# Kernel optimization log

Measured on AMD Instinct MI355X. Metric: run time of the kernel, lower is better.

## Reference

```python
import jax, jax.numpy as jnp
import numpy as np

N = 100000      # nodes
E = 1600000     # edges
D_IN, D_H, D_OUT = 256, 64, 47


def setup_inputs() -> dict:
    key = jax.random.key(0)
    k0, k1, k2, k3 = jax.random.split(key, 4)
    x = jax.random.normal(k0, (N, D_IN), dtype=jnp.float32)
    edge_index = jax.random.randint(k1, (2, E), 0, N, dtype=jnp.int64)
    W1 = jax.random.normal(k2, (D_IN, D_H), dtype=jnp.float32) / np.sqrt(D_IN)
    b1 = jnp.zeros((D_H,), dtype=jnp.float32)
    W2 = jax.random.normal(k3, (D_H, D_OUT), dtype=jnp.float32) / np.sqrt(D_H)
    b2 = jnp.zeros((D_OUT,), dtype=jnp.float32)
    return {"x": x, "edge_index": edge_index, "W1": W1, "b1": b1, "W2": W2, "b2": b2}


def _gcn_conv(x, W, b, src, dst, norm):
    # PyG GCNConv: h = x @ W, then scatter_add(norm * h[src] -> dst), + bias
    h = x @ W                                     # [N, out]
    msg = norm[:, None] * h[src]                  # [E+N, out] gather
    out = jax.ops.segment_sum(msg, dst, num_segments=N)  # scatter-add
    return out + b


def reference(x, edge_index, W1, b1, W2, b2):
    # add self-loops with weight 1 (PyG default, edge_weight=None -> ones)
    loop = jnp.arange(N, dtype=edge_index.dtype)
    src = jnp.concatenate([edge_index[0], loop])
    dst = jnp.concatenate([edge_index[1], loop])
    w = jnp.ones((E + N,), dtype=x.dtype)
    # symmetric normalization: deg^-1/2[src] * w * deg^-1/2[dst]
    deg = jax.ops.segment_sum(w, dst, num_segments=N)
    dinv = jnp.where(deg > 0, jax.lax.rsqrt(deg), 0.0)
    norm = dinv[src] * w * dinv[dst]              # [E+N]

    h = _gcn_conv(x, W1, b1, src, dst, norm)
    h = jax.nn.relu(h)
    # F.dropout(training=self.training): eval mode -> identity
    xo = _gcn_conv(h, W2, b2, src, dst, norm)     # [N, D_OUT]
    logits = jax.nn.softmax(xo, axis=1)           # nn.Softmax() -> dim=1 for 2D
    preds = jnp.argmax(logits, axis=1)
    return (logits, preds, xo)
```

## Files before the change

kernel.cpp:

```cpp
#include <hip/hip_runtime.h>
#include <math.h>

#define NN 100000
#define NE 1600000
#define DI 256
#define DH 64
#define DO 47
#define DH3 48
#define NB ((NN + 255) / 256)
#define RSZ8 ((NN + 7) / 8)
#define EPB 2048
#define CPB ((NE + EPB - 1) / EPB)

typedef float f8 __attribute__((ext_vector_type(8)));

__global__ __launch_bounds__(256) void k_degree(const int* __restrict__ dst,
                                                int* __restrict__ deg) {
    int r = blockIdx.x & 7;
    int chunk = blockIdx.x >> 3;
    int lo = r * RSZ8, hi = min(lo + RSZ8, NN);
    int base = chunk * EPB + threadIdx.x;
    #pragma unroll
    for (int i = 0; i < EPB / 256; ++i) {
        int e = base + i * 256;
        if (e < NE) {
            int d = dst[e];
            if (d >= lo && d < hi) atomicAdd(&deg[d], 1);
        }
    }
}

__global__ __launch_bounds__(256) void k_part(const int* __restrict__ deg,
                                              int* __restrict__ part) {
    int i = blockIdx.x * 256 + threadIdx.x;
    int v = (i < NN) ? deg[i] : 0;
    for (int off = 32; off; off >>= 1) v += __shfl_xor(v, off);
    __shared__ int s[4];
    if ((threadIdx.x & 63) == 0) s[threadIdx.x >> 6] = v;
    __syncthreads();
    if (threadIdx.x == 0) part[blockIdx.x] = s[0] + s[1] + s[2] + s[3];
}

__global__ __launch_bounds__(512) void k_scanpart(int* __restrict__ part) {
    int t = threadIdx.x, lane = t & 63, wv = t >> 6;
    int v0 = (t < NB) ? part[t] : 0;
    int v = v0;
    for (int off = 1; off < 64; off <<= 1) {
        int u = __shfl_up(v, off);
        if (lane >= off) v += u;
    }
    __shared__ int ws[8];
    if (lane == 63) ws[wv] = v;
    __syncthreads();
    if (t == 0) {
        int run = 0;
        for (int w = 0; w < 8; ++w) { int tmp = ws[w]; ws[w] = run; run += tmp; }
    }
    __syncthreads();
    v += ws[wv];
    if (t < NB) part[t] = v - v0;
}

__global__ __launch_bounds__(256) void k_scan3(const int* __restrict__ deg,
                                               const int* __restrict__ part,
                                               int* __restrict__ rowptr,
                                               int* __restrict__ cursor,
                                               float* __restrict__ dinv) {
    int i = blockIdx.x * 256 + threadIdx.x;
    int lane = threadIdx.x & 63, wv = threadIdx.x >> 6;
    int v0 = (i < NN) ? deg[i] : 0;
    int v = v0;
    for (int off = 1; off < 64; off <<= 1) {
        int u = __shfl_up(v, off);
        if (lane >= off) v += u;
    }
    __shared__ int ws[4], wo[4];
    if (lane == 63) ws[wv] = v;
    __syncthreads();
    if (threadIdx.x == 0) {
        int run = 0;
        for (int w = 0; w < 4; ++w) { int tmp = ws[w]; wo[w] = run; run += tmp; }
    }
    __syncthreads();
    int excl = part[blockIdx.x] + wo[wv] + v - v0;
    if (i < NN) {
        rowptr[i] = excl;
        cursor[i] = excl;
        dinv[i] = rsqrtf((float)(v0 + 1));
    }
}

__global__ __launch_bounds__(256) void k_fillr(const int* __restrict__ src,
                                               const int* __restrict__ dst,
                                               int* __restrict__ cursor,
                                               int* __restrict__ csr_src) {
    int r = blockIdx.x & 7;
    int chunk = blockIdx.x >> 3;
    int lo = r * RSZ8, hi = min(lo + RSZ8, NN);
    int base = chunk * EPB + threadIdx.x;
    #pragma unroll
    for (int i = 0; i < EPB / 256; ++i) {
        int e = base + i * 256;
        if (e < NE) {
            int d = dst[e];
            if (d >= lo && d < hi) {
                int p = atomicAdd(&cursor[d], 1);
                csr_src[p] = src[e];
            }
        }
    }
}

__global__ __launch_bounds__(512) void k_gemm1(const float* __restrict__ x,
                                               const float* __restrict__ W1,
                                               const float* __restrict__ dinv,
                                               float* __restrict__ h1s) {
    __shared__ float xs[2][64 * 33];
    const int t = threadIdx.x;
    const int lane = t & 63;
    const int wvu = __builtin_amdgcn_readfirstlane(t >> 6);
    const int r0 = blockIdx.x * 64;
    const int sr = t >> 3;
    const int sk = (t & 7) * 4;
    const long xrow = (long)min(r0 + sr, NN - 1) * DI;
    const int row = r0 + lane;

    float acc[8] = {0.f, 0.f, 0.f, 0.f, 0.f, 0.f, 0.f, 0.f};

    {
        float4 v = *(const float4*)(x + xrow + sk);
        float* p = &xs[0][sr * 33 + sk];
        p[0] = v.x; p[1] = v.y; p[2] = v.z; p[3] = v.w;
    }
    __syncthreads();
    for (int c = 0; c < 8; ++c) {
        const int buf = c & 1;
        if (c + 1 < 8) {
            float4 v = *(const float4*)(x + xrow + (c + 1) * 32 + sk);
            float* p = &xs[buf ^ 1][sr * 33 + sk];
            p[0] = v.x; p[1] = v.y; p[2] = v.z; p[3] = v.w;
        }
        const f8* wp = (const f8*)(W1) + (size_t)(c * 32) * (DH / 8) + wvu;
        #pragma unroll
        for (int k = 0; k < 32; ++k) {
            float xv = xs[buf][lane * 33 + k];
            f8 w8 = wp[(size_t)k * (DH / 8)];
            #pragma unroll
            for (int j = 0; j < 8; ++j) acc[j] += w8[j] * xv;
        }
        __syncthreads();
    }
    if (row < NN) {
        float di = dinv[row];
        float4 o0 = {di * acc[0], di * acc[1], di * acc[2], di * acc[3]};
        float4 o1 = {di * acc[4], di * acc[5], di * acc[6], di * acc[7]};
        float4* hp = (float4*)(h1s + (long)row * DH + wvu * 8);
        hp[0] = o0;
        hp[1] = o1;
    }
}

__global__ __launch_bounds__(256) void k_agg1(const int* __restrict__ rowptr,
                                              const int* __restrict__ deg,
                                              const int* __restrict__ csr_src,
                                              const float* __restrict__ dinv,
                                              const float* __restrict__ h1s,
                                              const float* __restrict__ b1,
                                              const float* __restrict__ W2,
                                              float* __restrict__ h3s) {
    __shared__ float w2[DH * DO];
    __shared__ float sh[8][DH];
    for (int i = threadIdx.x; i < DH * DO; i += 256) w2[i] = W2[i];
    __syncthreads();
    const int wv = threadIdx.x >> 6, lane = threadIdx.x & 63;
    const int rA = blockIdx.x * 8 + wv * 2;
    const int rB = rA + 1;
    const int begA = rowptr[rA], cntA = deg[rA];
    const int begB = rowptr[rB], cntB = deg[rB];
    float accA = 0.f, accB = 0.f;
    const int tmax = max(cntA, cntB);
    #pragma unroll 2
    for (int j = 0; j < tmax; j += 4) {
        #pragma unroll
        for (int k = 0; k < 4; ++k) {
            int sa = csr_src[min(begA + j + k, NE - 1)];
            int sb = csr_src[min(begB + j + k, NE - 1)];
            float va = h1s[(size_t)sa * DH + lane];
            float vb = h1s[(size_t)sb * DH + lane];
            accA += (j + k < cntA) ? va : 0.f;
            accB += (j + k < cntB) ? vb : 0.f;
        }
    }
    const float diA = dinv[rA], diB = dinv[rB];
    float vA = diA * (accA + h1s[(size_t)rA * DH + lane]) + b1[lane];
    float vB = diB * (accB + h1s[(size_t)rB * DH + lane]) + b1[lane];
    sh[wv * 2 + 0][lane] = fmaxf(vA, 0.f);
    sh[wv * 2 + 1][lane] = fmaxf(vB, 0.f);
    __syncthreads();
    if (lane < DO) {
        float oA = 0.f, oB = 0.f;
        #pragma unroll 8
        for (int k = 0; k < DH; ++k) {
            float w = w2[k * DO + lane];
            oA += sh[wv * 2 + 0][k] * w;
            oB += sh[wv * 2 + 1][k] * w;
        }
        h3s[(size_t)rA * DH3 + lane] = diA * oA;
        h3s[(size_t)rB * DH3 + lane] = diB * oB;
    }
}

__global__ __launch_bounds__(256) void k_agg2(const int* __restrict__ rowptr,
                                              const int* __restrict__ deg,
                                              const int* __restrict__ csr_src,
                                              const float* __restrict__ dinv,
                                              const float* __restrict__ h3s,
                                              const float* __restrict__ b2,
                                              float* __restrict__ logits,
                                              float* __restrict__ preds,
                                              float* __restrict__ xo) {
    const int wv = threadIdx.x >> 6, lane = threadIdx.x & 63;
    const int rA = blockIdx.x * 8 + wv * 2;
    const int rB = rA + 1;
    const int begA = rowptr[rA], cntA = deg[rA];
    const int begB = rowptr[rB], cntB = deg[rB];
    const bool act = lane < DO;
    const int lx = act ? lane : 0;
    float accA = 0.f, accB = 0.f;
    const int tmax = max(cntA, cntB);
    #pragma unroll 2
    for (int j = 0; j < tmax; j += 4) {
        #pragma unroll
        for (int k = 0; k < 4; ++k) {
            int sa = csr_src[min(begA + j + k, NE - 1)];
            int sb = csr_src[min(begB + j + k, NE - 1)];
            float va = h3s[(size_t)sa * DH3 + lx];
            float vb = h3s[(size_t)sb * DH3 + lx];
            accA += (j + k < cntA) ? va : 0.f;
            accB += (j + k < cntB) ? vb : 0.f;
        }
    }
    const float diA = dinv[rA], diB = dinv[rB];
    float valA = -INFINITY, valB = -INFINITY;
    if (act) {
        valA = diA * (accA + h3s[(size_t)rA * DH3 + lane]) + b2[lane];
        valB = diB * (accB + h3s[(size_t)rB * DH3 + lane]) + b2[lane];
        xo[(size_t)rA * DO + lane] = valA;
        xo[(size_t)rB * DO + lane] = valB;
    }
    float mA = valA, mB = valB;
    for (int off = 32; off; off >>= 1) {
        mA = fmaxf(mA, __shfl_xor(mA, off));
        mB = fmaxf(mB, __shfl_xor(mB, off));
    }
    int idxA = (act && valA == mA) ? lane : (1 << 30);
    int idxB = (act && valB == mB) ? lane : (1 << 30);
    for (int off = 32; off; off >>= 1) {
        idxA = min(idxA, __shfl_xor(idxA, off));
        idxB = min(idxB, __shfl_xor(idxB, off));
    }
    float evA = act ? expf(valA - mA) : 0.f;
    float evB = act ? expf(valB - mB) : 0.f;
    float sA = evA, sB = evB;
    for (int off = 32; off; off >>= 1) {
        sA += __shfl_xor(sA, off);
        sB += __shfl_xor(sB, off);
    }
    if (act) {
        logits[(size_t)rA * DO + lane] = evA / sA;
        logits[(size_t)rB * DO + lane] = evB / sB;
    }
    if (lane == 0) {
        preds[rA] = (float)idxA;
        preds[rB] = (float)idxB;
    }
}

extern "C" void kernel_launch(void* const* d_in, const int* in_sizes, int n_in,
                              void* d_out, int out_size, void* d_ws, size_t ws_size,
                              hipStream_t stream) {
    const float* x  = (const float*)d_in[0];
    const int*   ei = (const int*)d_in[1];
    const float* W1 = (const float*)d_in[2];
    const float* b1 = (const float*)d_in[3];
    const float* W2 = (const float*)d_in[4];
    const float* b2 = (const float*)d_in[5];
    const int* src = ei;
    const int* dst = ei + NE;

    float* out    = (float*)d_out;
    float* logits = out;
    float* preds  = out + (size_t)NN * DO;
    float* xo     = preds + NN;

    char* wsb = (char*)d_ws;
    int*   deg     = (int*)wsb;                         wsb += (size_t)NN * 4;
    float* dinv    = (float*)wsb;                       wsb += (size_t)NN * 4;
    int*   rowptr  = (int*)wsb;                         wsb += (size_t)NN * 4;
    int*   cursor  = (int*)wsb;                         wsb += (size_t)NN * 4;
    int*   part    = (int*)wsb;                         wsb += (size_t)512 * 4;
    int*   csr_src = (int*)wsb;                         wsb += (size_t)NE * 4;
    float* h1s     = (float*)wsb;                       wsb += (size_t)NN * DH * 4;
    float* h3s     = (float*)wsb;                       wsb += (size_t)NN * DH3 * 4;

    hipMemsetAsync(deg, 0, NN * sizeof(int), stream);

    k_degree<<<8 * CPB, 256, 0, stream>>>(dst, deg);
    k_part<<<NB, 256, 0, stream>>>(deg, part);
    k_scanpart<<<1, 512, 0, stream>>>(part);
    k_scan3<<<NB, 256, 0, stream>>>(deg, part, rowptr, cursor, dinv);
    k_fillr<<<8 * CPB, 256, 0, stream>>>(src, dst, cursor, csr_src);
    k_gemm1<<<(NN + 63) / 64, 512, 0, stream>>>(x, W1, dinv, h1s);
    k_agg1<<<NN / 8, 256, 0, stream>>>(rowptr, deg, csr_src, dinv, h1s, b1, W2, h3s);
    k_agg2<<<NN / 8, 256, 0, stream>>>(rowptr, deg, csr_src, dinv, h3s, b2, logits, preds, xo);
}
```

Measured before the change: 347.0 us.

## Stage W1 tiles in LDS and process four rows per wave in aggregations

The GEMM kernel now double-buffers 32x64 tiles of W1 in shared memory alongside the x tiles, replacing per-wave global vector loads of the weights. The two aggregation kernels now handle four destination rows per wave instead of two, which puts more independent gathers in flight and amortizes the per-block W2 staging over more rows. The costs are extra LDS use, higher register pressure and more load imbalance between rows of different degree within a wave.

```diff
diff --git a/kernel.cpp b/kernel.cpp
--- a/kernel.cpp
+++ b/kernel.cpp
@@ -116,12 +116,15 @@
                                                const float* __restrict__ dinv,
                                                float* __restrict__ h1s) {
     __shared__ float xs[2][64 * 33];
+    __shared__ float wl[2][32 * 64];
     const int t = threadIdx.x;
     const int lane = t & 63;
     const int wvu = __builtin_amdgcn_readfirstlane(t >> 6);
     const int r0 = blockIdx.x * 64;
     const int sr = t >> 3;
     const int sk = (t & 7) * 4;
+    const int wk = t >> 4;
+    const int wc = (t & 15) * 4;
     const long xrow = (long)min(r0 + sr, NN - 1) * DI;
     const int row = r0 + lane;
 
@@ -131,6 +134,9 @@
         float4 v = *(const float4*)(x + xrow + sk);
         float* p = &xs[0][sr * 33 + sk];
         p[0] = v.x; p[1] = v.y; p[2] = v.z; p[3] = v.w;
+        float4 w = *(const float4*)(W1 + (size_t)wk * DH + wc);
+        float* q = &wl[0][wk * 64 + wc];
+        q[0] = w.x; q[1] = w.y; q[2] = w.z; q[3] = w.w;
     }
     __syncthreads();
     for (int c = 0; c < 8; ++c) {
@@ -139,12 +145,14 @@
             float4 v = *(const float4*)(x + xrow + (c + 1) * 32 + sk);
             float* p = &xs[buf ^ 1][sr * 33 + sk];
             p[0] = v.x; p[1] = v.y; p[2] = v.z; p[3] = v.w;
-        }
-        const f8* wp = (const f8*)(W1) + (size_t)(c * 32) * (DH / 8) + wvu;
+            float4 w = *(const float4*)(W1 + (size_t)((c + 1) * 32 + wk) * DH + wc);
+            float* q = &wl[buf ^ 1][wk * 64 + wc];
+            q[0] = w.x; q[1] = w.y; q[2] = w.z; q[3] = w.w;
+        }
         #pragma unroll
         for (int k = 0; k < 32; ++k) {
             float xv = xs[buf][lane * 33 + k];
-            f8 w8 = wp[(size_t)k * (DH / 8)];
+            f8 w8 = *(const f8*)&wl[buf][k * 64 + wvu * 8];
             #pragma unroll
             for (int j = 0; j < 8; ++j) acc[j] += w8[j] * xv;
         }
@@ -169,44 +177,49 @@
                                               const float* __restrict__ W2,
                                               float* __restrict__ h3s) {
     __shared__ float w2[DH * DO];
-    __shared__ float sh[8][DH];
+    __shared__ float sh[16][DH];
     for (int i = threadIdx.x; i < DH * DO; i += 256) w2[i] = W2[i];
     __syncthreads();
     const int wv = threadIdx.x >> 6, lane = threadIdx.x & 63;
-    const int rA = blockIdx.x * 8 + wv * 2;
-    const int rB = rA + 1;
-    const int begA = rowptr[rA], cntA = deg[rA];
-    const int begB = rowptr[rB], cntB = deg[rB];
-    float accA = 0.f, accB = 0.f;
-    const int tmax = max(cntA, cntB);
-    #pragma unroll 2
+    const int rbase = blockIdx.x * 16 + wv * 4;
+    int beg[4], cnt[4];
+    float acc[4] = {0.f, 0.f, 0.f, 0.f};
+    #pragma unroll
+    for (int r = 0; r < 4; ++r) {
+        beg[r] = rowptr[rbase + r];
+        cnt[r] = deg[rbase + r];
+    }
+    const int tmax = max(max(cnt[0], cnt[1]), max(cnt[2], cnt[3]));
     for (int j = 0; j < tmax; j += 4) {
         #pragma unroll
         for (int k = 0; k < 4; ++k) {
-            int sa = csr_src[min(begA + j + k, NE - 1)];
-            int sb = csr_src[min(begB + j + k, NE - 1)];
-            float va = h1s[(size_t)sa * DH + lane];
-            float vb = h1s[(size_t)sb * DH + lane];
-            accA += (j + k < cntA) ? va : 0.f;
-            accB += (j + k < cntB) ? vb : 0.f;
-        }
-    }
-    const float diA = dinv[rA], diB = dinv[rB];
-    float vA = diA * (accA + h1s[(size_t)rA * DH + lane]) + b1[lane];
-    float vB = diB * (accB + h1s[(size_t)rB * DH + lane]) + b1[lane];
-    sh[wv * 2 + 0][lane] = fmaxf(vA, 0.f);
-    sh[wv * 2 + 1][lane] = fmaxf(vB, 0.f);
+            #pragma unroll
+            for (int r = 0; r < 4; ++r) {
+                int s = csr_src[min(beg[r] + j + k, NE - 1)];
+                float v = h1s[(size_t)s * DH + lane];
+                acc[r] += (j + k < cnt[r]) ? v : 0.f;
+            }
+        }
+    }
+    float di[4];
+    #pragma unroll
+    for (int r = 0; r < 4; ++r) {
+        di[r] = dinv[rbase + r];
+        float v = di[r] * (acc[r] + h1s[(size_t)(rbase + r) * DH + lane]) + b1[lane];
+        sh[wv * 4 + r][lane] = fmaxf(v, 0.f);
+    }
     __syncthreads();
     if (lane < DO) {
-        float oA = 0.f, oB = 0.f;
+        float o[4] = {0.f, 0.f, 0.f, 0.f};
         #pragma unroll 8
         for (int k = 0; k < DH; ++k) {
             float w = w2[k * DO + lane];
-            oA += sh[wv * 2 + 0][k] * w;
-            oB += sh[wv * 2 + 1][k] * w;
-        }
-        h3s[(size_t)rA * DH3 + lane] = diA * oA;
-        h3s[(size_t)rB * DH3 + lane] = diB * oB;
+            #pragma unroll
+            for (int r = 0; r < 4; ++r) o[r] += sh[wv * 4 + r][k] * w;
+        }
+        #pragma unroll
+        for (int r = 0; r < 4; ++r)
+            h3s[(size_t)(rbase + r) * DH3 + lane] = di[r] * o[r];
     }
 }
 
@@ -220,59 +233,63 @@
                                               float* __restrict__ preds,
                                               float* __restrict__ xo) {
     const int wv = threadIdx.x >> 6, lane = threadIdx.x & 63;
-    const int rA = blockIdx.x * 8 + wv * 2;
-    const int rB = rA + 1;
-    const int begA = rowptr[rA], cntA = deg[rA];
-    const int begB = rowptr[rB], cntB = deg[rB];
+    const int rbase = blockIdx.x * 16 + wv * 4;
     const bool act = lane < DO;
     const int lx = act ? lane : 0;
-    float accA = 0.f, accB = 0.f;
-    const int tmax = max(cntA, cntB);
-    #pragma unroll 2
+    int beg[4], cnt[4];
+    float acc[4] = {0.f, 0.f, 0.f, 0.f};
+    #pragma unroll
+    for (int r = 0; r < 4; ++r) {
+        beg[r] = rowptr[rbase + r];
+        cnt[r] = deg[rbase + r];
+    }
+    const int tmax = max(max(cnt[0], cnt[1]), max(cnt[2], cnt[3]));
     for (int j = 0; j < tmax; j += 4) {
         #pragma unroll
         for (int k = 0; k < 4; ++k) {
-            int sa = csr_src[min(begA + j + k, NE - 1)];
-            int sb = csr_src[min(begB + j + k, NE - 1)];
-            float va = h3s[(size_t)sa * DH3 + lx];
-            float vb = h3s[(size_t)sb * DH3 + lx];
-            accA += (j + k < cntA) ? va : 0.f;
-            accB += (j + k < cntB) ? vb : 0.f;
-        }
-    }
-    const float diA = dinv[rA], diB = dinv[rB];
-    float valA = -INFINITY, valB = -INFINITY;
+            #pragma unroll
+            for (int r = 0; r < 4; ++r) {
+                int s = csr_src[min(beg[r] + j + k, NE - 1)];
+                float v = h3s[(size_t)s * DH3 + lx];
+                acc[r] += (j + k < cnt[r]) ? v : 0.f;
+            }
+        }
+    }
+    float val[4];
+    #pragma unroll
+    for (int r = 0; r < 4; ++r) {
+        float di = dinv[rbase + r];
+        val[r] = act ? di * (acc[r] + h3s[(size_t)(rbase + r) * DH3 + lane]) + b2[lane]
+                     : -INFINITY;
+        if (act) xo[(size_t)(rbase + r) * DO + lane] = val[r];
+    }
+    float m[4] = {val[0], val[1], val[2], val[3]};
+    for (int off = 32; off; off >>= 1) {
+        #pragma unroll
+        for (int r = 0; r < 4; ++r) m[r] = fmaxf(m[r], __shfl_xor(m[r], off));
+    }
+    int idx[4];
+    #pragma unroll
+    for (int r = 0; r < 4; ++r) idx[r] = (act && val[r] == m[r]) ? lane : (1 << 30);
+    for (int off = 32; off; off >>= 1) {
+        #pragma unroll
+        for (int r = 0; r < 4; ++r) idx[r] = min(idx[r], __shfl_xor(idx[r], off));
+    }
+    float ev[4], ss[4];
+    #pragma unroll
+    for (int r = 0; r < 4; ++r) { ev[r] = act ? expf(val[r] - m[r]) : 0.f; ss[r] = ev[r]; }
+    for (int off = 32; off; off >>= 1) {
+        #pragma unroll
+        for (int r = 0; r < 4; ++r) ss[r] += __shfl_xor(ss[r], off);
+    }
     if (act) {
-        valA = diA * (accA + h3s[(size_t)rA * DH3 + lane]) + b2[lane];
-        valB = diB * (accB + h3s[(size_t)rB * DH3 + lane]) + b2[lane];
-        xo[(size_t)rA * DO + lane] = valA;
-        xo[(size_t)rB * DO + lane] = valB;
-    }
-    float mA = valA, mB = valB;
-    for (int off = 32; off; off >>= 1) {
-        mA = fmaxf(mA, __shfl_xor(mA, off));
-        mB = fmaxf(mB, __shfl_xor(mB, off));
-    }
-    int idxA = (act && valA == mA) ? lane : (1 << 30);
-    int idxB = (act && valB == mB) ? lane : (1 << 30);
-    for (int off = 32; off; off >>= 1) {
-        idxA = min(idxA, __shfl_xor(idxA, off));
-        idxB = min(idxB, __shfl_xor(idxB, off));
-    }
-    float evA = act ? expf(valA - mA) : 0.f;
-    float evB = act ? expf(valB - mB) : 0.f;
-    float sA = evA, sB = evB;
-    for (int off = 32; off; off >>= 1) {
-        sA += __shfl_xor(sA, off);
-        sB += __shfl_xor(sB, off);
-    }
-    if (act) {
-        logits[(size_t)rA * DO + lane] = evA / sA;
-        logits[(size_t)rB * DO + lane] = evB / sB;
+        #pragma unroll
+        for (int r = 0; r < 4; ++r)
+            logits[(size_t)(rbase + r) * DO + lane] = ev[r] / ss[r];
     }
     if (lane == 0) {
-        preds[rA] = (float)idxA;
-        preds[rB] = (float)idxB;
+        #pragma unroll
+        for (int r = 0; r < 4; ++r) preds[rbase + r] = (float)idx[r];
     }
 }
 
@@ -311,6 +328,6 @@
     k_scan3<<<NB, 256, 0, stream>>>(deg, part, rowptr, cursor, dinv);
     k_fillr<<<8 * CPB, 256, 0, stream>>>(src, dst, cursor, csr_src);
     k_gemm1<<<(NN + 63) / 64, 512, 0, stream>>>(x, W1, dinv, h1s);
-    k_agg1<<<NN / 8, 256, 0, stream>>>(rowptr, deg, csr_src, dinv, h1s, b1, W2, h3s);
-    k_agg2<<<NN / 8, 256, 0, stream>>>(rowptr, deg, csr_src, dinv, h3s, b2, logits, preds, xo);
-}
+    k_agg1<<<NN / 16, 256, 0, stream>>>(rowptr, deg, csr_src, dinv, h1s, b1, W2, h3s);
+    k_agg2<<<NN / 16, 256, 0, stream>>>(rowptr, deg, csr_src, dinv, h3s, b2, logits, preds, xo);
+}
```

After: 453.4 us. +30.7%, slower.
